# Optimization experiments

Hardware: AMD Instinct MI355X
Metric: run time of the kernel (lower is better)

The kernel has to match this reference:

```python
import jax, jax.numpy as jnp
import numpy as np

EMBED_DIM = 1024
NUM_HEADS = 16
HEAD_DIM = EMBED_DIM // NUM_HEADS
SCALE = HEAD_DIM ** (-0.5)


def setup_inputs() -> dict:
    key = jax.random.key(0)
    ks = jax.random.split(key, 13)
    B, N, D = 4, 4096, EMBED_DIM
    lin_scale = 1.0 / np.sqrt(D)
    inp = {
        "q": jax.random.normal(ks[0], (B, N, D), dtype=jnp.float32),
        "k": jax.random.normal(ks[1], (B, N, D), dtype=jnp.float32),
        "v": jax.random.normal(ks[2], (B, N, D), dtype=jnp.float32),
        "Wq": jax.random.uniform(ks[3], (D, D), jnp.float32, -lin_scale, lin_scale),
        "bq": jax.random.uniform(ks[4], (D,), jnp.float32, -lin_scale, lin_scale),
        "Wk": jax.random.uniform(ks[5], (D, D), jnp.float32, -lin_scale, lin_scale),
        "bk": jax.random.uniform(ks[6], (D,), jnp.float32, -lin_scale, lin_scale),
        "Wv": jax.random.uniform(ks[7], (D, D), jnp.float32, -lin_scale, lin_scale),
        "bv": jax.random.uniform(ks[8], (D,), jnp.float32, -lin_scale, lin_scale),
        "q_alpha": jax.random.normal(ks[9], (NUM_HEADS, HEAD_DIM), dtype=jnp.float32),
        "k_beta": jax.random.normal(ks[10], (NUM_HEADS, HEAD_DIM), dtype=jnp.float32),
        "Wo": jax.random.uniform(ks[11], (D, D), jnp.float32, -lin_scale, lin_scale),
        "bo": jax.random.uniform(ks[12], (D,), jnp.float32, -lin_scale, lin_scale),
    }
    return inp


def reference(q, k, v, Wq, bq, Wk, bk, Wv, bv, q_alpha, k_beta, Wo, bo):
    B, N, D = q.shape
    H, Dh = NUM_HEADS, HEAD_DIM
    # torch Linear: x @ W.T + b
    Q = (q @ Wq.T + bq).reshape(B, N, H, Dh)
    K = (k @ Wk.T + bk).reshape(B, N, H, Dh)
    V = (v @ Wv.T + bv).reshape(B, N, H, Dh)
    # alpha: [B,N,H] -> softmax over N
    alpha = jnp.einsum('bnhd,hd->bnh', Q, q_alpha) * SCALE
    alpha = jax.nn.softmax(alpha, axis=1)
    # global_q: [B,1,H,Dh]
    global_q = jnp.einsum('bnhd,bnh->bhd', Q, alpha)[:, None]
    P = K * global_q  # [B,N,H,Dh]
    beta = jnp.einsum('bnhd,hd->bnh', P, k_beta) * SCALE
    beta = jax.nn.softmax(beta, axis=1)
    global_v = jnp.einsum('bnhd,bnh->bhd', V, beta)[:, None]
    out = (Q + global_v).reshape(B, N, D)
    out = out @ Wo.T + bo
    return out
```

## Files before the change

### kernel.cpp

```cpp
#include <hip/hip_runtime.h>
#include <hip/hip_bf16.h>
#include <cstdint>
#include <cstddef>

#define SEQ    4096
#define NB     4
#define DIM    1024
#define NHEAD  16
#define HDIM   64
#define MROWS  (NB * SEQ)
#define SCALEF 0.125f
#define NT     16

typedef short          s16x8 __attribute__((ext_vector_type(8)));
typedef unsigned short u16x8 __attribute__((ext_vector_type(8)));
typedef float          f32x4 __attribute__((ext_vector_type(4)));
typedef unsigned short u16;

__device__ __forceinline__ u16 f2bf(float f) {
  return __builtin_bit_cast(u16, __float2bfloat16(f));
}
__device__ __forceinline__ float bf2f(u16 u) {
  return __builtin_bit_cast(float, (uint32_t)u << 16);
}
__device__ __forceinline__ void gload_lds16(const void* g, void* l) {
  __builtin_amdgcn_global_load_lds(
      (const __attribute__((address_space(1))) void*)g,
      (__attribute__((address_space(3))) void*)l, 16, 0, 0);
}

__global__ __launch_bounds__(256) void cvt_weights(
    const float* __restrict__ w0, const float* __restrict__ w1,
    const float* __restrict__ w2, const float* __restrict__ w3,
    u16* __restrict__ o0, u16* __restrict__ o1,
    u16* __restrict__ o2, u16* __restrict__ o3)
{
  int t = blockIdx.x * 256 + threadIdx.x;
  int m = t >> 17;
  int off = (t & 131071) * 8;
  const float* s = (m == 0) ? w0 : (m == 1) ? w1 : (m == 2) ? w2 : w3;
  u16*         d = (m == 0) ? o0 : (m == 1) ? o1 : (m == 2) ? o2 : o3;
  float4 a = ((const float4*)(s + off))[0];
  float4 b = ((const float4*)(s + off))[1];
  u16x8 p;
  p[0] = f2bf(a.x); p[1] = f2bf(a.y); p[2] = f2bf(a.z); p[3] = f2bf(a.w);
  p[4] = f2bf(b.x); p[5] = f2bf(b.y); p[6] = f2bf(b.z); p[7] = f2bf(b.w);
  *(u16x8*)(d + off) = p;
}

__global__ __launch_bounds__(256) void cvt_act(
    const float* __restrict__ s, u16* __restrict__ d)
{
  int t = blockIdx.x * 256 + threadIdx.x;
  int off = t * 8;
  float4 a = ((const float4*)(s + off))[0];
  float4 b = ((const float4*)(s + off))[1];
  u16x8 p;
  p[0] = f2bf(a.x); p[1] = f2bf(a.y); p[2] = f2bf(a.z); p[3] = f2bf(a.w);
  p[4] = f2bf(b.x); p[5] = f2bf(b.y); p[6] = f2bf(b.z); p[7] = f2bf(b.w);
  *(u16x8*)(d + off) = p;
}

template<int MODE>
__global__ __launch_bounds__(512) void gemm256(
    const u16* __restrict__ A, const u16* __restrict__ W,
    const float* __restrict__ bias, u16* __restrict__ Cb, float* __restrict__ Cf,
    const float* __restrict__ c2, int do_alpha,
    const float* __restrict__ qalpha, float* __restrict__ la)
{
  extern __shared__ __align__(16) char smem[];
  const int tid = threadIdx.x;
  const int lane = tid & 63, wave = tid >> 6;
  const int wr = wave >> 2, wc = wave & 3;
  const int fr = lane & 15, fq = lane >> 4;
  const int m0 = blockIdx.x * 256, n0 = blockIdx.y * 256;
  const int wrow = wr * 128, wcol = wc * 64;

  const int arow = tid >> 3;
  const int scol = (((tid & 7) ^ ((tid >> 3) & 7)) * 8);

  f32x4 acc[8][4];
  #pragma unroll
  for (int i = 0; i < 8; ++i)
    #pragma unroll
    for (int j = 0; j < 4; ++j) acc[i][j] = (f32x4){0.f, 0.f, 0.f, 0.f};

  auto stA = [&](int kt, int h) {
    const u16* g = A + (size_t)(m0 + h * 128) * DIM + kt * 64;
    char* l = smem + (kt & 1) * 32768 + h * 16384;
    gload_lds16(g + (size_t)arow * DIM + scol,        l + tid * 16);
    gload_lds16(g + (size_t)(64 + arow) * DIM + scol, l + 8192 + tid * 16);
  };
  auto stB = [&](int kt, int h) {
    const u16* g = W + (size_t)(n0 + h * 128) * DIM + kt * 64;
    char* l = smem + 65536 + (kt & 1) * 32768 + h * 16384;
    gload_lds16(g + (size_t)arow * DIM + scol,        l + tid * 16);
    gload_lds16(g + (size_t)(64 + arow) * DIM + scol, l + 8192 + tid * 16);
  };
  auto ldsoff = [&](int R, int ks) -> size_t {
    return (size_t)R * 128 + (size_t)((ks * 64 + fq * 16) ^ ((R & 7) << 4));
  };

  stA(0, 0); stA(0, 1); stB(0, 0); stB(0, 1);
  stA(1, 0);
  asm volatile("s_waitcnt vmcnt(2)" ::: "memory");
  asm volatile("s_barrier" ::: "memory");

  for (int t = 0; t < NT; ++t) {
    const char* Abase = smem + (t & 1) * 32768;
    const char* Bbase = smem + 65536 + (t & 1) * 32768;
    s16x8 areg[4][2];
    s16x8 breg_all[4][2];
    #pragma unroll
    for (int p = 0; p < 4; ++p) {
      const int mq = p >> 1, nq = p & 1;
      if (p == 0) {
        #pragma unroll
        for (int nj = 0; nj < 4; ++nj)
          #pragma unroll
          for (int ks = 0; ks < 2; ++ks)
            breg_all[nj][ks] = *(const s16x8*)(Bbase + ldsoff(wcol + nj * 16 + fr, ks));
      }
      if (nq == 0) {
        #pragma unroll
        for (int i = 0; i < 4; ++i)
          #pragma unroll
          for (int ks = 0; ks < 2; ++ks)
            areg[i][ks] = *(const s16x8*)(Abase + ldsoff(wrow + (mq * 4 + i) * 16 + fr, ks));
      }
      if (p == 0 && t + 1 < NT) stA(t + 1, 1);
      if (p == 1 && t + 1 < NT) stB(t + 1, 0);
      if (p == 2 && t + 1 < NT) stB(t + 1, 1);
      if (p == 3 && t + 2 < NT) stA(t + 2, 0);

      asm volatile("s_barrier" ::: "memory");
      __builtin_amdgcn_s_setprio(1);
      #pragma unroll
      for (int i = 0; i < 4; ++i)
        #pragma unroll
        for (int j = 0; j < 2; ++j)
          #pragma unroll
          for (int ks = 0; ks < 2; ++ks)
            acc[mq * 4 + i][nq * 2 + j] = __builtin_amdgcn_mfma_f32_16x16x32_bf16(
                areg[i][ks], breg_all[nq * 2 + j][ks], acc[mq * 4 + i][nq * 2 + j], 0, 0, 0);
      __builtin_amdgcn_s_setprio(0);
      if (p < 3) {
        asm volatile("s_barrier" ::: "memory");
      } else {
        if (t == NT - 2) asm volatile("s_waitcnt vmcnt(0)" ::: "memory");
        else             asm volatile("s_waitcnt vmcnt(2)" ::: "memory");
        asm volatile("s_barrier" ::: "memory");
      }
    }
  }

  if constexpr (MODE == 0) {
    #pragma unroll
    for (int ni = 0; ni < 4; ++ni) {
      const int col = n0 + wcol + ni * 16 + fr;
      const float bvv = bias[col];
      #pragma unroll
      for (int mi = 0; mi < 8; ++mi)
        #pragma unroll
        for (int r = 0; r < 4; ++r)
          acc[mi][ni][r] += bvv;
    }
    #pragma unroll
    for (int ni = 0; ni < 4; ++ni) {
      const int col = n0 + wcol + ni * 16 + fr;
      #pragma unroll
      for (int mi = 0; mi < 8; ++mi) {
        #pragma unroll
        for (int r = 0; r < 4; ++r) {
          const int row = m0 + wrow + mi * 16 + fq * 4 + r;
          Cb[(size_t)row * DIM + col] = f2bf(acc[mi][ni][r]);
        }
      }
    }
    if (do_alpha) {
      const int h = (n0 >> 6) + wc;
      float qa0 = qalpha[h * HDIM + 0 * 16 + fr];
      float qa1 = qalpha[h * HDIM + 1 * 16 + fr];
      float qa2 = qalpha[h * HDIM + 2 * 16 + fr];
      float qa3 = qalpha[h * HDIM + 3 * 16 + fr];
      #pragma unroll
      for (int mi = 0; mi < 8; ++mi) {
        #pragma unroll
        for (int r = 0; r < 4; ++r) {
          float p = acc[mi][0][r] * qa0 + acc[mi][1][r] * qa1
                  + acc[mi][2][r] * qa2 + acc[mi][3][r] * qa3;
          p += __shfl_xor(p, 1);
          p += __shfl_xor(p, 2);
          p += __shfl_xor(p, 4);
          p += __shfl_xor(p, 8);
          if (fr == 0) {
            const int row = m0 + wrow + mi * 16 + fq * 4 + r;
            la[((size_t)(row >> 12) * NHEAD + h) * SEQ + (row & (SEQ - 1))] = p * SCALEF;
          }
        }
      }
    }
  } else {
    const int bidx = m0 >> 12;
    #pragma unroll
    for (int ni = 0; ni < 4; ++ni) {
      const int col = n0 + wcol + ni * 16 + fr;
      const float cv = c2[bidx * DIM + col];
      #pragma unroll
      for (int mi = 0; mi < 8; ++mi) {
        #pragma unroll
        for (int r = 0; r < 4; ++r) {
          const int row = m0 + wrow + mi * 16 + fq * 4 + r;
          Cf[(size_t)row * DIM + col] = acc[mi][ni][r] + cv;
        }
      }
    }
  }
}

__global__ __launch_bounds__(256) void softmax_norm(
    float* __restrict__ l, float* __restrict__ zbuf)
{
  const int bh = blockIdx.x;
  const int tid = threadIdx.x, lane = tid & 63, wave = tid >> 6;
  float* p = l + (size_t)bh * SEQ;
  __shared__ float red[8];

  float4 v[4];
  #pragma unroll
  for (int i = 0; i < 4; ++i) v[i] = ((const float4*)p)[i * 256 + tid];

  float m = -1e30f;
  #pragma unroll
  for (int i = 0; i < 4; ++i)
    m = fmaxf(m, fmaxf(fmaxf(v[i].x, v[i].y), fmaxf(v[i].z, v[i].w)));
  #pragma unroll
  for (int o = 32; o; o >>= 1) m = fmaxf(m, __shfl_xor(m, o));
  if (lane == 0) red[wave] = m;
  __syncthreads();
  m = fmaxf(fmaxf(red[0], red[1]), fmaxf(red[2], red[3]));

  float s = 0.f;
  #pragma unroll
  for (int i = 0; i < 4; ++i) {
    v[i].x = __expf(v[i].x - m); v[i].y = __expf(v[i].y - m);
    v[i].z = __expf(v[i].z - m); v[i].w = __expf(v[i].w - m);
    s += (v[i].x + v[i].y) + (v[i].z + v[i].w);
  }
  #pragma unroll
  for (int o = 32; o; o >>= 1) s += __shfl_xor(s, o);
  if (lane == 0) red[4 + wave] = s;
  __syncthreads();
  s = (red[4] + red[5]) + (red[6] + red[7]);

  float inv = 1.0f / s;
  #pragma unroll
  for (int i = 0; i < 4; ++i) {
    v[i].x *= inv; v[i].y *= inv; v[i].z *= inv; v[i].w *= inv;
    ((float4*)p)[i * 256 + tid] = v[i];
  }
  if (tid < HDIM) zbuf[bh * HDIM + tid] = 0.f;
}

__global__ __launch_bounds__(256) void accum_weighted(
    const u16* __restrict__ X, const float* __restrict__ w,
    float* __restrict__ outp)
{
  const int bh = blockIdx.y, chunk = blockIdx.x;
  const int b = bh >> 4, h = bh & 15;
  const int tid = threadIdx.x, lane = tid & 63, wave = tid >> 6;
  const int rsub = lane >> 3, cl = lane & 7;
  const size_t base = (size_t)b * SEQ * DIM + h * HDIM;
  const int n0 = chunk * 512;

  float acc[8] = {0, 0, 0, 0, 0, 0, 0, 0};
  for (int it = 0; it < 16; ++it) {
    int n = n0 + it * 32 + wave * 8 + rsub;
    u16x8 u = *(const u16x8*)(X + base + (size_t)n * DIM + cl * 8);
    float wv = w[(size_t)bh * SEQ + n];
    #pragma unroll
    for (int j = 0; j < 8; ++j) acc[j] += wv * bf2f(u[j]);
  }
  #pragma unroll
  for (int j = 0; j < 8; ++j) {
    acc[j] += __shfl_xor(acc[j], 8);
    acc[j] += __shfl_xor(acc[j], 16);
    acc[j] += __shfl_xor(acc[j], 32);
  }
  __shared__ float part[4][64];
  if (rsub == 0) {
    #pragma unroll
    for (int j = 0; j < 8; ++j) part[wave][cl * 8 + j] = acc[j];
  }
  __syncthreads();
  if (tid < HDIM) {
    float s = (part[0][tid] + part[1][tid]) + (part[2][tid] + part[3][tid]);
    atomicAdd(&outp[bh * HDIM + tid], s);
  }
}

__global__ __launch_bounds__(256) void logits_beta(
    const u16* __restrict__ Kb, const float* __restrict__ gq,
    const float* __restrict__ kbeta, float* __restrict__ lb)
{
  __shared__ float vb[NHEAD][HDIM];
  const int rg = blockIdx.x;
  const int b = rg >> 8;
  const int tid = threadIdx.x, lane = tid & 63, wave = tid >> 6;

  for (int i = tid; i < NHEAD * HDIM; i += 256)
    ((float*)vb)[i] = gq[b * DIM + i] * kbeta[i] * SCALEF;
  __syncthreads();

  const int h = lane >> 2, dq = (lane & 3) * 16;
  #pragma unroll
  for (int i = 0; i < 4; ++i) {
    int gr = rg * 16 + wave * 4 + i;
    const u16* rp = Kb + (size_t)gr * DIM + h * HDIM + dq;
    u16x8 u0 = *(const u16x8*)rp;
    u16x8 u1 = *(const u16x8*)(rp + 8);
    float dot = 0.f;
    #pragma unroll
    for (int j = 0; j < 8; ++j) dot += bf2f(u0[j]) * vb[h][dq + j];
    #pragma unroll
    for (int j = 0; j < 8; ++j) dot += bf2f(u1[j]) * vb[h][dq + 8 + j];
    dot += __shfl_xor(dot, 1);
    dot += __shfl_xor(dot, 2);
    if ((lane & 3) == 0) {
      lb[((size_t)b * NHEAD + h) * SEQ + (gr & (SEQ - 1))] = dot;
    }
  }
}

__global__ __launch_bounds__(256) void gv_wo_kernel(
    const float* __restrict__ gv, const float* __restrict__ Wo,
    const float* __restrict__ bo, float* __restrict__ c2)
{
  int wid = blockIdx.x * 4 + (threadIdx.x >> 6);
  int b = wid >> 10, j = wid & 1023;
  int lane = threadIdx.x & 63;
  float acc = 0.f;
  #pragma unroll
  for (int c = 0; c < 16; ++c) {
    int kk = c * 64 + lane;
    acc += gv[b * DIM + kk] * Wo[(size_t)j * DIM + kk];
  }
  #pragma unroll
  for (int o = 32; o; o >>= 1) acc += __shfl_down(acc, o);
  if (lane == 0) c2[wid] = acc + bo[j];
}

extern "C" void kernel_launch(void* const* d_in, const int* in_sizes, int n_in,
                              void* d_out, int out_size, void* d_ws, size_t ws_size,
                              hipStream_t stream) {
  const float* q  = (const float*)d_in[0];
  const float* k  = (const float*)d_in[1];
  const float* v  = (const float*)d_in[2];
  const float* Wq = (const float*)d_in[3];
  const float* bq = (const float*)d_in[4];
  const float* Wk = (const float*)d_in[5];
  const float* bk = (const float*)d_in[6];
  const float* Wv = (const float*)d_in[7];
  const float* bv = (const float*)d_in[8];
  const float* qa = (const float*)d_in[9];
  const float* kb = (const float*)d_in[10];
  const float* Wo = (const float*)d_in[11];
  const float* bo = (const float*)d_in[12];
  float* out = (float*)d_out;

  u16* Qb  = (u16*)d_ws;
  u16* Kb  = Qb + (size_t)MROWS * DIM;
  u16* Vb  = Kb + (size_t)MROWS * DIM;
  u16* Wqb = Vb + (size_t)MROWS * DIM;
  u16* Wkb = Wqb + (size_t)DIM * DIM;
  u16* Wvb = Wkb + (size_t)DIM * DIM;
  u16* Wob = Wvb + (size_t)DIM * DIM;
  float* la   = (float*)(Wob + (size_t)DIM * DIM);
  float* lb   = la + (size_t)NB * NHEAD * SEQ;
  float* gq   = lb + (size_t)NB * NHEAD * SEQ;
  float* gv   = gq + NB * DIM;
  float* c2   = gv + NB * DIM;

  u16* actb = (u16*)d_out;

  const dim3 g256(MROWS / 256, DIM / 256);
  const size_t ldsb = 131072;

  cvt_weights<<<2048, 256, 0, stream>>>(Wq, Wk, Wv, Wo, Wqb, Wkb, Wvb, Wob);

  cvt_act<<<8192, 256, 0, stream>>>(q, actb);
  gemm256<0><<<g256, 512, ldsb, stream>>>(actb, Wqb, bq, Qb, nullptr, nullptr, 1, qa, la);
  cvt_act<<<8192, 256, 0, stream>>>(k, actb);
  gemm256<0><<<g256, 512, ldsb, stream>>>(actb, Wkb, bk, Kb, nullptr, nullptr, 0, qa, la);
  cvt_act<<<8192, 256, 0, stream>>>(v, actb);
  gemm256<0><<<g256, 512, ldsb, stream>>>(actb, Wvb, bv, Vb, nullptr, nullptr, 0, qa, la);

  softmax_norm<<<64, 256, 0, stream>>>(la, gq);
  accum_weighted<<<dim3(8, 64), 256, 0, stream>>>(Qb, la, gq);
  logits_beta<<<1024, 256, 0, stream>>>(Kb, gq, kb, lb);
  softmax_norm<<<64, 256, 0, stream>>>(lb, gv);
  accum_weighted<<<dim3(8, 64), 256, 0, stream>>>(Vb, lb, gv);
  gv_wo_kernel<<<1024, 256, 0, stream>>>(gv, Wo, bo, c2);
  gemm256<1><<<g256, 512, ldsb, stream>>>(Qb, Wob, nullptr, nullptr, out, c2, 0, qa, la);
}
```

Baseline: 246.2 us.

## Fuse fp32-to-bf16 activation conversion into projection GEMM A-tile loads

After: 260.0 us. 5.6% more time.

```diff
diff --git a/kernel.cpp b/kernel.cpp
--- a/kernel.cpp
+++ b/kernel.cpp
@@ -48,25 +48,13 @@
   *(u16x8*)(d + off) = p;
 }
 
-__global__ __launch_bounds__(256) void cvt_act(
-    const float* __restrict__ s, u16* __restrict__ d)
-{
-  int t = blockIdx.x * 256 + threadIdx.x;
-  int off = t * 8;
-  float4 a = ((const float4*)(s + off))[0];
-  float4 b = ((const float4*)(s + off))[1];
-  u16x8 p;
-  p[0] = f2bf(a.x); p[1] = f2bf(a.y); p[2] = f2bf(a.z); p[3] = f2bf(a.w);
-  p[4] = f2bf(b.x); p[5] = f2bf(b.y); p[6] = f2bf(b.z); p[7] = f2bf(b.w);
-  *(u16x8*)(d + off) = p;
-}
-
-template<int MODE>
+template<int MODE, int AF32>
 __global__ __launch_bounds__(512) void gemm256(
     const u16* __restrict__ A, const u16* __restrict__ W,
     const float* __restrict__ bias, u16* __restrict__ Cb, float* __restrict__ Cf,
     const float* __restrict__ c2, int do_alpha,
-    const float* __restrict__ qalpha, float* __restrict__ la)
+    const float* __restrict__ qalpha, float* __restrict__ la,
+    const float* __restrict__ Af)
 {
   extern __shared__ __align__(16) char smem[];
   const int tid = threadIdx.x;
@@ -77,7 +65,8 @@
   const int wrow = wr * 128, wcol = wc * 64;
 
   const int arow = tid >> 3;
-  const int scol = (((tid & 7) ^ ((tid >> 3) & 7)) * 8);
+  const int acnk = tid & 7;
+  const int scol = ((acnk ^ (arow & 7)) * 8);
 
   f32x4 acc[8][4];
   #pragma unroll
@@ -97,13 +86,44 @@
     gload_lds16(g + (size_t)arow * DIM + scol,        l + tid * 16);
     gload_lds16(g + (size_t)(64 + arow) * DIM + scol, l + 8192 + tid * 16);
   };
+  auto ldA4 = [&](int kt, int h, f32x4* r) {
+    const float* g = Af + (size_t)(m0 + h * 128 + arow) * DIM + kt * 64 + acnk * 8;
+    r[0] = *(const f32x4*)g;
+    r[1] = *(const f32x4*)(g + 4);
+    const float* g2 = g + (size_t)64 * DIM;
+    r[2] = *(const f32x4*)g2;
+    r[3] = *(const f32x4*)(g2 + 4);
+  };
+  auto wrA = [&](int kt, int h, const f32x4* r) {
+    char* l = smem + (kt & 1) * 32768 + h * 16384;
+    const int wb = arow * 128 + ((acnk ^ (arow & 7)) << 4);
+    u16x8 p0, p1;
+    #pragma unroll
+    for (int j = 0; j < 4; ++j) { p0[j] = f2bf(r[0][j]); p0[4 + j] = f2bf(r[1][j]); }
+    #pragma unroll
+    for (int j = 0; j < 4; ++j) { p1[j] = f2bf(r[2][j]); p1[4 + j] = f2bf(r[3][j]); }
+    *(u16x8*)(l + wb) = p0;
+    *(u16x8*)(l + 8192 + wb) = p1;
+  };
   auto ldsoff = [&](int R, int ks) -> size_t {
     return (size_t)R * 128 + (size_t)((ks * 64 + fq * 16) ^ ((R & 7) << 4));
   };
 
-  stA(0, 0); stA(0, 1); stB(0, 0); stB(0, 1);
-  stA(1, 0);
-  asm volatile("s_waitcnt vmcnt(2)" ::: "memory");
+  f32x4 rA0[4], rA1[4], r00[4], r01[4];
+
+  if constexpr (AF32) {
+    ldA4(0, 0, r00); ldA4(0, 1, r01);
+    stB(0, 0); stB(0, 1);
+    ldA4(1, 0, rA0);
+    asm volatile("s_waitcnt vmcnt(8)" ::: "memory");
+    wrA(0, 0, r00); wrA(0, 1, r01);
+    asm volatile("s_waitcnt vmcnt(4)" ::: "memory");
+    asm volatile("s_waitcnt lgkmcnt(0)" ::: "memory");
+  } else {
+    stA(0, 0); stA(0, 1); stB(0, 0); stB(0, 1);
+    stA(1, 0);
+    asm volatile("s_waitcnt vmcnt(2)" ::: "memory");
+  }
   asm volatile("s_barrier" ::: "memory");
 
   for (int t = 0; t < NT; ++t) {
@@ -128,10 +148,25 @@
           for (int ks = 0; ks < 2; ++ks)
             areg[i][ks] = *(const s16x8*)(Abase + ldsoff(wrow + (mq * 4 + i) * 16 + fr, ks));
       }
-      if (p == 0 && t + 1 < NT) stA(t + 1, 1);
-      if (p == 1 && t + 1 < NT) stB(t + 1, 0);
-      if (p == 2 && t + 1 < NT) stB(t + 1, 1);
-      if (p == 3 && t + 2 < NT) stA(t + 2, 0);
+      if constexpr (AF32) {
+        if (p == 0 && t + 1 < NT) ldA4(t + 1, 1, rA1);
+        if (p == 1 && t + 1 < NT) {
+          asm volatile("s_waitcnt vmcnt(4)" ::: "memory");
+          wrA(t + 1, 0, rA0);
+          stB(t + 1, 0);
+        }
+        if (p == 2 && t + 1 < NT) {
+          asm volatile("s_waitcnt vmcnt(2)" ::: "memory");
+          wrA(t + 1, 1, rA1);
+          stB(t + 1, 1);
+        }
+        if (p == 3 && t + 2 < NT) ldA4(t + 2, 0, rA0);
+      } else {
+        if (p == 0 && t + 1 < NT) stA(t + 1, 1);
+        if (p == 1 && t + 1 < NT) stB(t + 1, 0);
+        if (p == 2 && t + 1 < NT) stB(t + 1, 1);
+        if (p == 3 && t + 2 < NT) stA(t + 2, 0);
+      }
 
       asm volatile("s_barrier" ::: "memory");
       __builtin_amdgcn_s_setprio(1);
@@ -147,8 +182,16 @@
       if (p < 3) {
         asm volatile("s_barrier" ::: "memory");
       } else {
-        if (t == NT - 2) asm volatile("s_waitcnt vmcnt(0)" ::: "memory");
-        else             asm volatile("s_waitcnt vmcnt(2)" ::: "memory");
+        if constexpr (AF32) {
+          if (t + 1 < NT) {
+            if (t == NT - 2) asm volatile("s_waitcnt vmcnt(0)" ::: "memory");
+            else             asm volatile("s_waitcnt vmcnt(4)" ::: "memory");
+            asm volatile("s_waitcnt lgkmcnt(0)" ::: "memory");
+          }
+        } else {
+          if (t == NT - 2) asm volatile("s_waitcnt vmcnt(0)" ::: "memory");
+          else             asm volatile("s_waitcnt vmcnt(2)" ::: "memory");
+        }
         asm volatile("s_barrier" ::: "memory");
       }
     }
@@ -381,19 +424,17 @@
   float* gv   = gq + NB * DIM;
   float* c2   = gv + NB * DIM;
 
-  u16* actb = (u16*)d_out;
-
   const dim3 g256(MROWS / 256, DIM / 256);
   const size_t ldsb = 131072;
 
   cvt_weights<<<2048, 256, 0, stream>>>(Wq, Wk, Wv, Wo, Wqb, Wkb, Wvb, Wob);
 
-  cvt_act<<<8192, 256, 0, stream>>>(q, actb);
-  gemm256<0><<<g256, 512, ldsb, stream>>>(actb, Wqb, bq, Qb, nullptr, nullptr, 1, qa, la);
-  cvt_act<<<8192, 256, 0, stream>>>(k, actb);
-  gemm256<0><<<g256, 512, ldsb, stream>>>(actb, Wkb, bk, Kb, nullptr, nullptr, 0, qa, la);
-  cvt_act<<<8192, 256, 0, stream>>>(v, actb);
-  gemm256<0><<<g256, 512, ldsb, stream>>>(actb, Wvb, bv, Vb, nullptr, nullptr, 0, qa, la);
+  gemm256<0, 1><<<g256, 512, ldsb, stream>>>(nullptr, Wqb, bq, Qb, nullptr,
+                                             nullptr, 1, qa, la, q);
+  gemm256<0, 1><<<g256, 512, ldsb, stream>>>(nullptr, Wkb, bk, Kb, nullptr,
+                                             nullptr, 0, qa, la, k);
+  gemm256<0, 1><<<g256, 512, ldsb, stream>>>(nullptr, Wvb, bv, Vb, nullptr,
+                                             nullptr, 0, qa, la, v);
 
   softmax_norm<<<64, 256, 0, stream>>>(la, gq);
   accum_weighted<<<dim3(8, 64), 256, 0, stream>>>(Qb, la, gq);
@@ -401,5 +442,6 @@
   softmax_norm<<<64, 256, 0, stream>>>(lb, gv);
   accum_weighted<<<dim3(8, 64), 256, 0, stream>>>(Vb, lb, gv);
   gv_wo_kernel<<<1024, 256, 0, stream>>>(gv, Wo, bo, c2);
-  gemm256<1><<<g256, 512, ldsb, stream>>>(Qb, Wob, nullptr, nullptr, out, c2, 0, qa, la);
-}
+  gemm256<1, 0><<<g256, 512, ldsb, stream>>>(Qb, Wob, nullptr, nullptr, out,
+                                             c2, 0, qa, la, nullptr);
+}
```
